# Kernel tuning notes

Measured on AMD Instinct MI355X. Metric: run time of the kernel, lower is better.

The kernel has to match this reference:

```python
import jax, jax.numpy as jnp
from jax import lax
import numpy as np

N = 200000
H = 64          # h
C = 2 * H       # 2h feature channels
L = 128         # voxel grid side
KV = 125        # 5^3 kernel volume
KEEP = KV // 2 + 1  # 63 offsets kept by mask type 'B' (incl. center)


def _build_kernel_map(coords):
    # coords: [N,3] int voxel coords, unique. Returns nidx [KEEP, N] int32, -1 if no neighbor.
    keys = (coords[:, 0].astype(np.int64) * L + coords[:, 1]) * L + coords[:, 2]
    order = np.argsort(keys)
    skeys = keys[order]
    nidx = np.full((KEEP, N), -1, dtype=np.int32)
    for k in range(KEEP):
        dx, dy, dz = k // 25 - 2, (k // 5) % 5 - 2, k % 5 - 2
        nc = coords + np.array([dx, dy, dz])
        inb = np.all((nc >= 0) & (nc < L), axis=1)
        qk = (nc[:, 0].astype(np.int64) * L + nc[:, 1]) * L + nc[:, 2]
        pos = np.searchsorted(skeys, qk)
        posc = np.minimum(pos, N - 1)
        found = inb & (skeys[posc] == qk)
        nidx[k] = np.where(found, order[posc].astype(np.int32), -1)
    return nidx


def setup_inputs() -> dict:
    key = jax.random.key(0)
    k1, k2, k3, k4, k5 = jax.random.split(key, 5)
    rng = np.random.default_rng(0)
    flat = rng.choice(L ** 3, size=N, replace=False)
    coords = np.stack(np.unravel_index(flat, (L, L, L)), axis=1).astype(np.int32)
    nidx = jnp.asarray(_build_kernel_map(coords))
    s = 0.05
    return {
        "x_feats": jax.random.normal(k1, (N, C), jnp.float32),
        "y_feats": jax.random.normal(k2, (N, C), jnp.float32),
        "Wa": jax.random.normal(k3, (C, H), jnp.float32) * s,
        "Wb": jax.random.normal(k4, (KV, H, H), jnp.float32) * s,
        "Wc": jax.random.normal(k5, (H, C), jnp.float32) * s,
        "nidx": nidx,
    }


def reference(x_feats, y_feats, Wa, Wb, Wc, nidx):
    # mask type 'B': zero kernel offsets >= KV//2 + 1
    mask = (jnp.arange(KV) < KEEP)[:, None, None].astype(Wb.dtype)
    Wb_kept = (Wb * mask)[:KEEP]  # [KEEP, H, H]; remaining offsets contribute 0

    def block(f):
        f = jax.nn.elu(f)
        f = f @ Wa                      # 1x1 conv 2h->h
        f = jax.nn.elu(f)
        # masked sparse 5^3 conv: gather-GEMM-accumulate over kernel offsets
        def body(acc, kw):
            idx, W = kw                 # idx [N], W [H,H]
            g = jnp.where((idx >= 0)[:, None], f[jnp.maximum(idx, 0)], 0.0)
            return acc + g @ W, None
        acc0 = jnp.zeros((f.shape[0], H), f.dtype)
        f, _ = lax.scan(body, acc0, (nidx, Wb_kept))
        f = jax.nn.elu(f)
        return f @ Wc                   # 1x1 conv h->2h

    out = x_feats + y_feats
    return x_feats + block(out)
```

## Files before the change

kernel.cpp:

```cpp
#include <hip/hip_runtime.h>
#include <cmath>

#define N_PTS 200000
#define HD 64
#define CD 128
#define KEEP 63

typedef __bf16 bf16;
typedef __bf16 bf16x4 __attribute__((ext_vector_type(4)));
typedef __bf16 bf16x8 __attribute__((ext_vector_type(8)));
typedef float f32x4 __attribute__((ext_vector_type(4)));
typedef float f32x16 __attribute__((ext_vector_type(16)));

__device__ __forceinline__ float elu_f(float v) {
    return v > 0.f ? v : __expf(v) - 1.f;
}

__global__ __launch_bounds__(256) void k_prep(const float* __restrict__ Wb,
                                              const float* __restrict__ Wc,
                                              const float* __restrict__ Wa,
                                              bf16* __restrict__ WbT,
                                              bf16* __restrict__ WcT2,
                                              bf16* __restrict__ WaT,
                                              bf16* __restrict__ zp) {
    int idx = blockIdx.x * 256 + threadIdx.x;
    if (idx < KEEP * HD * HD) {
        int k = idx >> 12;
        int rem = idx & 4095;
        int o = rem >> 6, i = rem & 63;
        int dst = ((i >> 4) * 2 + (o >> 5)) * 512 +
                  (((i >> 3) & 1) * 32 + (o & 31)) * 8 + (i & 7);
        WbT[(k << 12) + dst] = (bf16)Wb[(k * HD + i) * HD + o];
        return;
    }
    int e = idx - KEEP * HD * HD;
    if (e < CD * HD) {
        int c = e >> 6, h = e & 63;
        int dst = ((c >> 5) * 4 + (h >> 4)) * 512 +
                  ((((h >> 3) & 1) * 32) + (c & 31)) * 8 + (h & 7);
        WcT2[dst] = (bf16)Wc[h * CD + c];
        return;
    }
    e -= CD * HD;
    if (e < HD * CD) {
        int o = e >> 7, c = e & 127;
        int dst = ((c >> 4) * 2 + (o >> 5)) * 512 +
                  (((c >> 3) & 1) * 32 + (o & 31)) * 8 + (c & 7);
        WaT[dst] = (bf16)Wa[c * HD + o];
        return;
    }
    e -= HD * CD;
    if (e < 64) zp[e] = (bf16)0.f;
}

__global__ __launch_bounds__(256, 4) void k_stage1(const float* __restrict__ x,
                                                   const float* __restrict__ y,
                                                   const bf16* __restrict__ WaT,
                                                   bf16* __restrict__ f) {
    __shared__ bf16 pbuf[4][32 * 64];
    int tid = threadIdx.x;
    int wave = tid >> 6;
    int lane = tid & 63;
    int l31 = lane & 31;
    int half = lane >> 5;
    int pbase_w = blockIdx.x * 128 + wave * 32;
    int p = pbase_w + l31;
    int pc = p < N_PTS ? p : N_PTS - 1;

    const float* xr = x + (size_t)pc * CD;
    const float* yr = y + (size_t)pc * CD;

    f32x16 acc[2];
#pragma unroll
    for (int mt = 0; mt < 2; mt++)
#pragma unroll
        for (int r = 0; r < 16; r++) acc[mt][r] = 0.f;

    f32x4 xa[2], xb[2], ya[2], yb[2];
    {
        int c0 = half * 8;
        xa[0] = *(const f32x4*)(xr + c0);
        xb[0] = *(const f32x4*)(xr + c0 + 4);
        ya[0] = *(const f32x4*)(yr + c0);
        yb[0] = *(const f32x4*)(yr + c0 + 4);
    }
#pragma unroll
    for (int ks = 0; ks < 8; ks++) {
        int cur = ks & 1, nxt = cur ^ 1;
        bf16x8 a0 = *(const bf16x8*)(WaT + (ks * 2 + 0) * 512 + lane * 8);
        bf16x8 a1 = *(const bf16x8*)(WaT + (ks * 2 + 1) * 512 + lane * 8);
        __builtin_amdgcn_sched_barrier(0);
        if (ks < 7) {
            int c0 = half * 8 + (ks + 1) * 16;
            xa[nxt] = *(const f32x4*)(xr + c0);
            xb[nxt] = *(const f32x4*)(xr + c0 + 4);
            ya[nxt] = *(const f32x4*)(yr + c0);
            yb[nxt] = *(const f32x4*)(yr + c0 + 4);
        }
        bf16x8 bv;
#pragma unroll
        for (int jj = 0; jj < 4; jj++) {
            bv[jj]     = (bf16)elu_f(xa[cur][jj] + ya[cur][jj]);
            bv[4 + jj] = (bf16)elu_f(xb[cur][jj] + yb[cur][jj]);
        }
        acc[0] = __builtin_amdgcn_mfma_f32_32x32x16_bf16(a0, bv, acc[0], 0, 0, 0);
        acc[1] = __builtin_amdgcn_mfma_f32_32x32x16_bf16(a1, bv, acc[1], 0, 0, 0);
        __builtin_amdgcn_sched_barrier(0);
    }

    bf16* pb = pbuf[wave];
#pragma unroll
    for (int mt = 0; mt < 2; mt++) {
#pragma unroll
        for (int q = 0; q < 4; q++) {
            bf16x4 v;
#pragma unroll
            for (int jj = 0; jj < 4; jj++)
                v[jj] = (bf16)elu_f(acc[mt][q * 4 + jj]);
            int chunk = mt * 4 + q;
            *(bf16x4*)&pb[l31 * 64 + ((chunk ^ (l31 & 7)) * 8) + 4 * half] = v;
        }
    }
#pragma unroll
    for (int qq = 0; qq < 4; qq++) {
        int t = lane + 64 * qq;
        int row = t >> 3, ch = t & 7;
        int pos = ch ^ (row & 7);
        bf16x8 v = *(const bf16x8*)&pb[row * 64 + pos * 8];
        int pp = pbase_w + row;
        if (pp < N_PTS)
            *(bf16x8*)(f + (size_t)pp * HD + ch * 8) = v;
    }
}

struct GR { bf16x8 v[4]; };
struct AF { bf16x8 v[8]; };

__global__ __launch_bounds__(256, 2) void k_conv(const bf16* __restrict__ f,
                                                 const int* __restrict__ nidx,
                                                 const bf16* __restrict__ WbT,
                                                 const bf16* __restrict__ WcT2,
                                                 const bf16* __restrict__ zp,
                                                 const float* __restrict__ x,
                                                 float* __restrict__ out) {
    __shared__ bf16 bounce[4][32 * 64];

    int tid = threadIdx.x;
    int wave = tid >> 6;
    int lane = tid & 63;
    int l31 = lane & 31;
    int half = lane >> 5;
    int g8 = lane >> 3;
    int l7 = lane & 7;
    int pbase = blockIdx.x * 128 + wave * 32;

    bf16* pb = bounce[wave];

    f32x16 acc[2];
#pragma unroll
    for (int mt = 0; mt < 2; mt++)
#pragma unroll
        for (int r = 0; r < 16; r++) acc[mt][r] = 0.f;

    auto ldidx4 = [&](int k, int i) -> int {
        int pp = pbase + i * 8 + g8;
        return (k < KEEP && pp < N_PTS) ? nidx[(size_t)k * N_PTS + pp] : -1;
    };
    auto gaddr = [&](int iv) -> const bf16* {
        return iv >= 0 ? f + (size_t)iv * HD + l7 * 8 : zp + l7 * 8;
    };
    auto gather4 = [&](GR& g, const int (&iv)[4]) {
#pragma unroll
        for (int i = 0; i < 4; i++)
            g.v[i] = *(const bf16x8*)gaddr(iv[i]);
    };
    auto dswrite = [&](const GR& g) {
#pragma unroll
        for (int i = 0; i < 4; i++) {
            int pp = i * 8 + g8;
            *(bf16x8*)&pb[pp * 64 + ((l7 ^ g8) * 8)] = g.v[i];
        }
    };
    auto loadA = [&](int k, AF& A) {
        const bf16* wk = WbT + ((size_t)k << 12);
#pragma unroll
        for (int fi = 0; fi < 8; fi++)
            A.v[fi] = *(const bf16x8*)(wk + fi * 512 + lane * 8);
    };
    auto mfma8 = [&](const AF& a) {
#pragma unroll
        for (int ks = 0; ks < 4; ks++) {
            int ci = ks * 2 + half;
            bf16x8 fb = *(const bf16x8*)&pb[l31 * 64 + ((ci ^ (l31 & 7)) * 8)];
            acc[0] = __builtin_amdgcn_mfma_f32_32x32x16_bf16(a.v[ks * 2 + 0], fb, acc[0], 0, 0, 0);
            acc[1] = __builtin_amdgcn_mfma_f32_32x32x16_bf16(a.v[ks * 2 + 1], fb, acc[1], 0, 0, 0);
        }
    };
    auto substep = [&](int k, GR& gfill, const GR& gwrite, int (&slot)[4]) {
        AF a;
        loadA(k, a);
        __builtin_amdgcn_sched_barrier(0);
        gather4(gfill, slot);
#pragma unroll
        for (int i = 0; i < 4; i++) slot[i] = ldidx4(k + 6, i);
        __builtin_amdgcn_sched_barrier(0);
        mfma8(a);
        __builtin_amdgcn_sched_barrier(0);
        dswrite(gwrite);
        __builtin_amdgcn_sched_barrier(0);
    };

    int s0[4], s1[4], s2[4], s3[4];
#pragma unroll
    for (int i = 0; i < 4; i++) s0[i] = ldidx4(2, i);
#pragma unroll
    for (int i = 0; i < 4; i++) s1[i] = ldidx4(3, i);
#pragma unroll
    for (int i = 0; i < 4; i++) s2[i] = ldidx4(4, i);
#pragma unroll
    for (int i = 0; i < 4; i++) s3[i] = ldidx4(5, i);
    GR ge, go;
    {
        int i0[4], i1[4];
#pragma unroll
        for (int i = 0; i < 4; i++) i0[i] = ldidx4(0, i);
#pragma unroll
        for (int i = 0; i < 4; i++) i1[i] = ldidx4(1, i);
        GR g0;
        gather4(g0, i0);
        gather4(go, i1);
        dswrite(g0);
    }

    for (int j = 0; j < 15; j++) {
        int k = 4 * j;
        substep(k,     ge, go, s0);
        substep(k + 1, go, ge, s1);
        substep(k + 2, ge, go, s2);
        substep(k + 3, go, ge, s3);
    }
    substep(60, ge, go, s0);
    substep(61, go, ge, s1);
    {
        AF a;
        loadA(62, a);
        mfma8(a);
    }

#pragma unroll
    for (int mt = 0; mt < 2; mt++) {
#pragma unroll
        for (int q = 0; q < 4; q++) {
            bf16x4 v;
#pragma unroll
            for (int jj = 0; jj < 4; jj++)
                v[jj] = (bf16)elu_f(acc[mt][q * 4 + jj]);
            int chunk = mt * 4 + q;
            *(bf16x4*)&pb[l31 * 64 + ((chunk ^ (l31 & 7)) * 8) + 4 * half] = v;
        }
    }
    bf16x8 pa[4];
#pragma unroll
    for (int ks = 0; ks < 4; ks++) {
        int ci = 2 * ks + half;
        pa[ks] = *(const bf16x8*)&pb[l31 * 64 + ((ci ^ (l31 & 7)) * 8)];
    }
#pragma unroll
    for (int ct = 0; ct < 4; ct++) {
        f32x16 o;
#pragma unroll
        for (int r = 0; r < 16; r++) o[r] = 0.f;
        int cc = ct * 32 + l31;
#pragma unroll
        for (int ks = 0; ks < 4; ks++) {
            bf16x8 bw = *(const bf16x8*)(WcT2 + ((ct * 4 + ks) << 9) + lane * 8);
            o = __builtin_amdgcn_mfma_f32_32x32x16_bf16(pa[ks], bw, o, 0, 0, 0);
        }
        int prow_base = pbase + 4 * half;
#pragma unroll
        for (int r = 0; r < 16; r++) {
            int prow = prow_base + (r & 3) + 8 * (r >> 2);
            if (prow < N_PTS) {
                size_t off = (size_t)prow * CD + cc;
                out[off] = x[off] + o[r];
            }
        }
    }
}

extern "C" void kernel_launch(void* const* d_in, const int* in_sizes, int n_in,
                              void* d_out, int out_size, void* d_ws, size_t ws_size,
                              hipStream_t stream) {
    const float* x  = (const float*)d_in[0];
    const float* y  = (const float*)d_in[1];
    const float* Wa = (const float*)d_in[2];
    const float* Wb = (const float*)d_in[3];
    const float* Wc = (const float*)d_in[4];
    const int* nidx = (const int*)d_in[5];
    float* out = (float*)d_out;

    char* ws = (char*)d_ws;
    bf16* f    = (bf16*)ws;
    bf16* WbT  = (bf16*)(ws + 25624576);
    bf16* WcT2 = (bf16*)(ws + 25624576 + 516096);
    bf16* WaT  = (bf16*)(ws + 25624576 + 516096 + 16384);
    bf16* zp   = (bf16*)(ws + 25624576 + 516096 + 16384 + 16384);

    k_prep<<<1073, 256, 0, stream>>>(Wb, Wc, Wa, WbT, WcT2, WaT, zp);
    k_stage1<<<1563, 256, 0, stream>>>(x, y, WaT, f);
    k_conv<<<1563, 256, 0, stream>>>(f, nidx, WbT, WcT2, zp, x, out);
}
```

Baseline: 539.5 us.

## Stage per-offset Wb tiles cooperatively into double-buffered LDS

Before, every wave loaded the full 64x64 bf16 weight tile for each kernel offset from global memory into registers. Now each wave loads one quarter of the next offset's tile and writes it into a double-buffered shared-memory area, and the MFMA loop reads its A fragments from LDS. This cuts redundant global/L2 weight traffic by four and frees registers. The cost is a block-wide barrier plus an lgkmcnt wait at every offset, and 16 KB more LDS per block, which could limit overlap or occupancy.

```diff
diff --git a/kernel.cpp b/kernel.cpp
--- a/kernel.cpp
+++ b/kernel.cpp
@@ -134,7 +134,6 @@
 }
 
 struct GR { bf16x8 v[4]; };
-struct AF { bf16x8 v[8]; };
 
 __global__ __launch_bounds__(256, 2) void k_conv(const bf16* __restrict__ f,
                                                  const int* __restrict__ nidx,
@@ -143,6 +142,7 @@
                                                  const bf16* __restrict__ zp,
                                                  const float* __restrict__ x,
                                                  float* __restrict__ out) {
+    __shared__ bf16 lds_a[2][4096];
     __shared__ bf16 bounce[4][32 * 64];
 
     int tid = threadIdx.x;
@@ -181,32 +181,42 @@
             *(bf16x8*)&pb[pp * 64 + ((l7 ^ g8) * 8)] = g.v[i];
         }
     };
-    auto loadA = [&](int k, AF& A) {
-        const bf16* wk = WbT + ((size_t)k << 12);
-#pragma unroll
-        for (int fi = 0; fi < 8; fi++)
-            A.v[fi] = *(const bf16x8*)(wk + fi * 512 + lane * 8);
-    };
-    auto mfma8 = [&](const AF& a) {
+    auto stageIssue = [&](int k, bf16x8& s0, bf16x8& s1) {
+        const bf16* wk = WbT + ((size_t)k << 12) + wave * 1024 + lane * 8;
+        s0 = *(const bf16x8*)(wk);
+        s1 = *(const bf16x8*)(wk + 512);
+    };
+    auto stageWrite = [&](int kb, const bf16x8& s0, const bf16x8& s1) {
+        bf16* d = &lds_a[kb][wave * 1024 + lane * 8];
+        *(bf16x8*)(d) = s0;
+        *(bf16x8*)(d + 512) = s1;
+    };
+    auto mfma8_lds = [&](int kb) {
+        const bf16* A = lds_a[kb];
 #pragma unroll
         for (int ks = 0; ks < 4; ks++) {
             int ci = ks * 2 + half;
             bf16x8 fb = *(const bf16x8*)&pb[l31 * 64 + ((ci ^ (l31 & 7)) * 8)];
-            acc[0] = __builtin_amdgcn_mfma_f32_32x32x16_bf16(a.v[ks * 2 + 0], fb, acc[0], 0, 0, 0);
-            acc[1] = __builtin_amdgcn_mfma_f32_32x32x16_bf16(a.v[ks * 2 + 1], fb, acc[1], 0, 0, 0);
+            bf16x8 a0 = *(const bf16x8*)&A[(ks * 2 + 0) * 512 + lane * 8];
+            bf16x8 a1 = *(const bf16x8*)&A[(ks * 2 + 1) * 512 + lane * 8];
+            acc[0] = __builtin_amdgcn_mfma_f32_32x32x16_bf16(a0, fb, acc[0], 0, 0, 0);
+            acc[1] = __builtin_amdgcn_mfma_f32_32x32x16_bf16(a1, fb, acc[1], 0, 0, 0);
         }
     };
     auto substep = [&](int k, GR& gfill, const GR& gwrite, int (&slot)[4]) {
-        AF a;
-        loadA(k, a);
+        bf16x8 sA0, sA1;
+        stageIssue(k + 1, sA0, sA1);
         __builtin_amdgcn_sched_barrier(0);
         gather4(gfill, slot);
 #pragma unroll
         for (int i = 0; i < 4; i++) slot[i] = ldidx4(k + 6, i);
         __builtin_amdgcn_sched_barrier(0);
-        mfma8(a);
+        mfma8_lds(k & 1);
         __builtin_amdgcn_sched_barrier(0);
         dswrite(gwrite);
+        stageWrite((k + 1) & 1, sA0, sA1);
+        asm volatile("s_waitcnt lgkmcnt(0)" ::: "memory");
+        __builtin_amdgcn_s_barrier();
         __builtin_amdgcn_sched_barrier(0);
     };
 
@@ -229,7 +239,13 @@
         GR g0;
         gather4(g0, i0);
         gather4(go, i1);
+        bf16x8 sA0, sA1;
+        stageIssue(0, sA0, sA1);
         dswrite(g0);
+        stageWrite(0, sA0, sA1);
+        asm volatile("s_waitcnt lgkmcnt(0)" ::: "memory");
+        __builtin_amdgcn_s_barrier();
+        __builtin_amdgcn_sched_barrier(0);
     }
 
     for (int j = 0; j < 15; j++) {
@@ -241,11 +257,7 @@
     }
     substep(60, ge, go, s0);
     substep(61, go, ge, s1);
-    {
-        AF a;
-        loadA(62, a);
-        mfma8(a);
-    }
+    mfma8_lds(0);
 
 #pragma unroll
     for (int mt = 0; mt < 2; mt++) {
```

Result: faster. 501.7 us (-7.0%).
